# Performance work log

Measured on AMD Instinct MI355X. Metric: run time of the kernel, lower is better.

## Reference

```python
import jax, jax.numpy as jnp
import numpy as np

H = 8
D_MODEL = 512
NEG = -1e9  # fp32 masking value from the torch source


def setup_inputs() -> dict:
    key = jax.random.key(0)
    ks = jax.random.split(key, 13)
    B, T, C, D = 2, 512, 8, D_MODEL
    s = 1.0 / np.sqrt(D)
    inp = {
        "query": jax.random.normal(ks[0], (B, T, C, D), jnp.float32),
        "key": jax.random.normal(ks[1], (B, T, C, D), jnp.float32),
        "value": jax.random.normal(ks[2], (B, T, C, D), jnp.float32),
        "mask": jax.random.randint(ks[3], (B, T, T, 1), 0, 2, jnp.int32),
        # four Linear(d_model, d_model) layers, stored as (in, out)
        "Wq": jax.random.normal(ks[4], (D, D), jnp.float32) * s,
        "bq": jax.random.normal(ks[5], (D,), jnp.float32) * s,
        "Wk": jax.random.normal(ks[6], (D, D), jnp.float32) * s,
        "bk": jax.random.normal(ks[7], (D,), jnp.float32) * s,
        "Wv": jax.random.normal(ks[8], (D, D), jnp.float32) * s,
        "bv": jax.random.normal(ks[9], (D,), jnp.float32) * s,
        "Wo": jax.random.normal(ks[10], (D, D), jnp.float32) * s,
        "bo": jax.random.normal(ks[11], (D,), jnp.float32) * s,
    }
    return inp


def _mha(query, key, value, mask, Wq, bq, Wk, bk, Wv, bv, Wo, bo):
    B, T, C, D = query.shape
    h, dk = H, D // H

    def proj(x, W, b):
        y = (x @ W + b).reshape(B, T, C, h, dk)
        return jnp.transpose(y, (0, 3, 2, 1, 4))  # [B,h,C,T,dk] (torch transpose(1,3))

    q = proj(query, Wq, bq)
    k = proj(key, Wk, bk)
    v = proj(value, Wv, bv)

    scores = jnp.einsum("bhctd,bhcsd->bhcts", q, k) / np.sqrt(dk)  # [B,h,C,T,T]
    # The torch view/transpose/view dance is just a permutation putting C last;
    # it is equivalent to masking scores[b,h,c,t,s] where mask[b,t,s,0]==0
    # (mask broadcast over heads h and channels c).
    m = mask[:, :, :, 0]  # [B,T,Tk]
    scores = jnp.where(m[:, None, None, :, :] == 0, NEG, scores)
    p_attn = jax.nn.softmax(scores, axis=-1)
    # dropout omitted (inference/deterministic reference)
    x = jnp.einsum("bhcts,bhcsd->bhctd", p_attn, v)  # [B,h,C,T,dk]
    x = jnp.transpose(x, (0, 3, 2, 1, 4)).reshape(B, T, C, D)
    return x @ Wo + bo


def reference(query, key, value, mask, Wq, bq, Wk, bk, Wv, bv, Wo, bo):
    return _mha(query, key, value, mask, Wq, bq, Wk, bk, Wv, bv, Wo, bo)
```

## Files before the change

### kernel.cpp

```cpp
#include <hip/hip_runtime.h>
#include <hip/hip_bf16.h>

typedef __bf16 bf16;
typedef __bf16 bf16x8 __attribute__((ext_vector_type(8)));
typedef float floatx4 __attribute__((ext_vector_type(4)));


#define AS1 __attribute__((address_space(1)))
#define AS3 __attribute__((address_space(3)))

__device__ __forceinline__ void gload_lds16(const bf16* g, bf16* l) {
    __builtin_amdgcn_global_load_lds((const AS1 unsigned int*)g,
                                     (AS3 unsigned int*)l, 16, 0, 0);
}

union Pack8 { bf16 h[8]; uint4 u; };

__global__ __launch_bounds__(256) void wtr_kernel(
    const float* __restrict__ Wq, const float* __restrict__ Wk,
    const float* __restrict__ Wv, const float* __restrict__ Wo,
    bf16* __restrict__ WT)
{
    __shared__ float Ts[64][65];
    const int tid = threadIdx.x;
    const int k0 = blockIdx.x * 64;
    const int n0 = blockIdx.y * 64;
    const int z  = blockIdx.z;
    const float* W = (z == 0) ? Wq : (z == 1) ? Wk : (z == 2) ? Wv : Wo;
    bf16* O = WT + (size_t)z * 512 * 512;
    #pragma unroll
    for (int i = 0; i < 16; i++) {
        const int r = i * 4 + (tid >> 6), c = tid & 63;
        Ts[r][c] = W[(size_t)(k0 + r) * 512 + n0 + c];
    }
    __syncthreads();
    #pragma unroll
    for (int i = 0; i < 16; i++) {
        const int a = i * 4 + (tid >> 6), c = tid & 63;
        O[(size_t)(n0 + a) * 512 + k0 + c] = (bf16)Ts[c][a];
    }
}

__global__ __launch_bounds__(256) void gemm_qkv(
    const float* __restrict__ Aq, const float* __restrict__ Ak,
    const float* __restrict__ Av, const bf16* __restrict__ WT,
    const float* __restrict__ Bq, const float* __restrict__ Bk,
    const float* __restrict__ Bv,
    bf16* __restrict__ Oq, bf16* __restrict__ Ok, bf16* __restrict__ Ov)
{
    __shared__ bf16 Asm[128 * 32];
    __shared__ bf16 Bsm[128 * 32];
    __shared__ bf16 Tsm[128][136];
    const int z = blockIdx.z;
    const float* A    = (z == 0) ? Aq : (z == 1) ? Ak : Av;
    const float* bias = (z == 0) ? Bq : (z == 1) ? Bk : Bv;
    bf16* out         = (z == 0) ? Oq : (z == 1) ? Ok : Ov;
    const bf16* BT = WT + (size_t)z * 262144;
    const float scale = (z == 0) ? 0.125f : 1.0f;

    const int tid  = threadIdx.x;
    const int lane = tid & 63;
    const int wave = tid >> 6;
    const int quad = lane >> 4;
    const int l16  = lane & 15;
    const int mblk = blockIdx.x * 128;
    const int nblk = blockIdx.y * 128;

    const int srow = wave * 16 + (lane >> 2);
    const int scol = (lane & 3) * 8;
    const float* Ag0 = A + (size_t)(mblk + srow) * 512 + scol;
    const float* Ag1 = Ag0 + (size_t)64 * 512;
    const bf16* Bg0 = BT + (size_t)(nblk + srow) * 512 + scol;
    const bf16* Bg1 = Bg0 + (size_t)64 * 512;
    bf16* Alp0 = Asm + srow * 32 + scol;
    bf16* Alp1 = Alp0 + 64 * 32;
    bf16* Bl0 = Bsm + wave * 16 * 32;
    bf16* Bl1 = Bsm + (64 + wave * 16) * 32;

    const int wr = (wave >> 1) * 64;
    const int wc = (wave & 1) * 64;

    floatx4 acc[4][4] = {};
    for (int k0 = 0; k0 < 512; k0 += 32) {
        gload_lds16(Bg0 + k0, Bl0);
        gload_lds16(Bg1 + k0, Bl1);
        float4 x0 = *(const float4*)(Ag0 + k0);
        float4 x1 = *(const float4*)(Ag0 + k0 + 4);
        float4 y0 = *(const float4*)(Ag1 + k0);
        float4 y1 = *(const float4*)(Ag1 + k0 + 4);
        Pack8 pa, pb;
        pa.h[0] = (bf16)x0.x; pa.h[1] = (bf16)x0.y;
        pa.h[2] = (bf16)x0.z; pa.h[3] = (bf16)x0.w;
        pa.h[4] = (bf16)x1.x; pa.h[5] = (bf16)x1.y;
        pa.h[6] = (bf16)x1.z; pa.h[7] = (bf16)x1.w;
        pb.h[0] = (bf16)y0.x; pb.h[1] = (bf16)y0.y;
        pb.h[2] = (bf16)y0.z; pb.h[3] = (bf16)y0.w;
        pb.h[4] = (bf16)y1.x; pb.h[5] = (bf16)y1.y;
        pb.h[6] = (bf16)y1.z; pb.h[7] = (bf16)y1.w;
        *(uint4*)Alp0 = pa.u;
        *(uint4*)Alp1 = pb.u;
        __syncthreads();
        bf16x8 a[4], b[4];
        #pragma unroll
        for (int mt = 0; mt < 4; mt++)
            a[mt] = *(const bf16x8*)(Asm + (wr + mt * 16 + l16) * 32 + quad * 8);
        #pragma unroll
        for (int nt = 0; nt < 4; nt++)
            b[nt] = *(const bf16x8*)(Bsm + (wc + nt * 16 + l16) * 32 + quad * 8);
        #pragma unroll
        for (int mt = 0; mt < 4; mt++)
            #pragma unroll
            for (int nt = 0; nt < 4; nt++)
                acc[mt][nt] = __builtin_amdgcn_mfma_f32_16x16x32_bf16(
                    a[mt], b[nt], acc[mt][nt], 0, 0, 0);
        __syncthreads();
    }

    if (z != 2) {
        #pragma unroll
        for (int mt = 0; mt < 4; mt++) {
            #pragma unroll
            for (int nt = 0; nt < 4; nt++) {
                const int colg = nblk + wc + nt * 16 + l16;
                const float bb = bias[colg];
                #pragma unroll
                for (int r = 0; r < 4; r++) {
                    const int rowg = mblk + wr + mt * 16 + quad * 4 + r;
                    const float v = (acc[mt][nt][r] + bb) * scale;
                    const int b_ = rowg >> 12;
                    const int t_ = (rowg >> 3) & 511;
                    const int c  = rowg & 7;
                    const int h  = colg >> 6;
                    const int d  = colg & 63;
                    const int hd = b_ * 64 + h * 8 + c;
                    out[((size_t)hd * 512 + t_) * 64 + d] = (bf16)v;
                }
            }
        }
    } else {
        #pragma unroll
        for (int mt = 0; mt < 4; mt++) {
            #pragma unroll
            for (int nt = 0; nt < 4; nt++) {
                const int cl = wc + nt * 16 + l16;
                const float bb = bias[nblk + cl];
                #pragma unroll
                for (int r = 0; r < 4; r++)
                    Tsm[wr + mt * 16 + quad * 4 + r][cl] =
                        (bf16)(acc[mt][nt][r] + bb);
            }
        }
        __syncthreads();
        const int b_ = mblk >> 12;
        const int t0 = (mblk >> 3) & 511;
        #pragma unroll
        for (int ch = tid; ch < 1024; ch += 256) {
            const int col = ch >> 3, c = ch & 7;
            const int h = (nblk + col) >> 6, d = (nblk + col) & 63;
            const int hd = b_ * 64 + h * 8 + c;
            Pack8 lo, hi;
            #pragma unroll
            for (int j = 0; j < 8; j++) lo.h[j] = Tsm[j * 8 + c][col];
            #pragma unroll
            for (int j = 0; j < 8; j++) hi.h[j] = Tsm[(j + 8) * 8 + c][col];
            bf16* dst = out + ((size_t)hd * 64 + d) * 512 + t0;
            *(uint4*)dst = lo.u;
            *(uint4*)(dst + 8) = hi.u;
        }
    }
}

__global__ __launch_bounds__(256) void gemm_o(
    const bf16* __restrict__ A, const bf16* __restrict__ BT,
    const float* __restrict__ bias, float* __restrict__ out)
{
    __shared__ bf16 Asm[128 * 32];
    __shared__ bf16 Bsm[128 * 32];
    const int tid  = threadIdx.x;
    const int lane = tid & 63;
    const int wave = tid >> 6;
    const int quad = lane >> 4;
    const int l16  = lane & 15;
    const int mblk = blockIdx.x * 128;
    const int nblk = blockIdx.y * 128;

    const int srow = wave * 16 + (lane >> 2);
    const int scol = (lane & 3) * 8;
    const bf16* Ag0 = A + (size_t)(mblk + srow) * 512 + scol;
    const bf16* Ag1 = Ag0 + (size_t)64 * 512;
    const bf16* Bg0 = BT + (size_t)(nblk + srow) * 512 + scol;
    const bf16* Bg1 = Bg0 + (size_t)64 * 512;
    bf16* Al0 = Asm + wave * 16 * 32;
    bf16* Al1 = Asm + (64 + wave * 16) * 32;
    bf16* Bl0 = Bsm + wave * 16 * 32;
    bf16* Bl1 = Bsm + (64 + wave * 16) * 32;

    const int wr = (wave >> 1) * 64;
    const int wc = (wave & 1) * 64;

    floatx4 acc[4][4] = {};
    for (int k0 = 0; k0 < 512; k0 += 32) {
        gload_lds16(Ag0 + k0, Al0);
        gload_lds16(Ag1 + k0, Al1);
        gload_lds16(Bg0 + k0, Bl0);
        gload_lds16(Bg1 + k0, Bl1);
        __syncthreads();
        bf16x8 a[4], b[4];
        #pragma unroll
        for (int mt = 0; mt < 4; mt++)
            a[mt] = *(const bf16x8*)(Asm + (wr + mt * 16 + l16) * 32 + quad * 8);
        #pragma unroll
        for (int nt = 0; nt < 4; nt++)
            b[nt] = *(const bf16x8*)(Bsm + (wc + nt * 16 + l16) * 32 + quad * 8);
        #pragma unroll
        for (int mt = 0; mt < 4; mt++)
            #pragma unroll
            for (int nt = 0; nt < 4; nt++)
                acc[mt][nt] = __builtin_amdgcn_mfma_f32_16x16x32_bf16(
                    a[mt], b[nt], acc[mt][nt], 0, 0, 0);
        __syncthreads();
    }

    #pragma unroll
    for (int mt = 0; mt < 4; mt++) {
        #pragma unroll
        for (int nt = 0; nt < 4; nt++) {
            const int colg = nblk + wc + nt * 16 + l16;
            const float bb = bias[colg];
            #pragma unroll
            for (int r = 0; r < 4; r++) {
                const int rowg = mblk + wr + mt * 16 + quad * 4 + r;
                out[(size_t)rowg * 512 + colg] = acc[mt][nt][r] + bb;
            }
        }
    }
}

#define PST 520

__global__ __launch_bounds__(256, 2) void attn_kernel(
    const bf16* __restrict__ Qws, const bf16* __restrict__ Kws,
    const bf16* __restrict__ Vtws, const int* __restrict__ mask,
    bf16* __restrict__ Xws)
{
    __shared__ bf16 Psm[64][PST];
    __shared__ float redM[4][64];
    __shared__ float redS[4][64];
    const int tid  = threadIdx.x;
    const int wave = tid >> 6;
    const int lane = tid & 63;
    const int quad = lane >> 4;
    const int l16  = lane & 15;
    const int s_ = blockIdx.x;
    const int o_ = ((s_ & 7) << 7) | (s_ >> 3);
    const int hd = o_ >> 3;
    const int qt = o_ & 7;
    const int q0 = qt * 64;
    const int b = hd >> 6;
    const int h = (hd >> 3) & 7;
    const int c = hd & 7;

    const bf16* Qh = Qws + (size_t)hd * 512 * 64;
    const bf16* Kh = Kws + (size_t)hd * 512 * 64;
    const int* mp = mask + ((size_t)b * 512 + q0) * 512;

    bf16x8 aq[4][2];
    #pragma unroll
    for (int s = 0; s < 4; s++) {
        aq[s][0] = *(const bf16x8*)(Qh + (size_t)(q0 + s * 16 + l16) * 64 + quad * 8);
        aq[s][1] = *(const bf16x8*)(Qh + (size_t)(q0 + s * 16 + l16) * 64 + 32 + quad * 8);
    }

    floatx4 sv[4][8];
    #pragma unroll
    for (int s = 0; s < 4; s++)
        #pragma unroll
        for (int nt = 0; nt < 8; nt++)
            sv[s][nt] = (floatx4){0.f, 0.f, 0.f, 0.f};

    #pragma unroll
    for (int nt = 0; nt < 8; nt++) {
        const int s0 = wave * 128 + nt * 16;
        bf16x8 bk0 = *(const bf16x8*)(Kh + (size_t)(s0 + l16) * 64 + quad * 8);
        bf16x8 bk1 = *(const bf16x8*)(Kh + (size_t)(s0 + l16) * 64 + 32 + quad * 8);
        #pragma unroll
        for (int s = 0; s < 4; s++) {
            sv[s][nt] = __builtin_amdgcn_mfma_f32_16x16x32_bf16(
                aq[s][0], bk0, sv[s][nt], 0, 0, 0);
            sv[s][nt] = __builtin_amdgcn_mfma_f32_16x16x32_bf16(
                aq[s][1], bk1, sv[s][nt], 0, 0, 0);
        }
    }

    float mx[4][4];
    #pragma unroll
    for (int s = 0; s < 4; s++)
        #pragma unroll
        for (int r = 0; r < 4; r++)
            mx[s][r] = -3.0e38f;
    #pragma unroll
    for (int s = 0; s < 4; s++)
        #pragma unroll
        for (int nt = 0; nt < 8; nt++)
            #pragma unroll
            for (int r = 0; r < 4; r++) {
                const int mv = mp[(size_t)(s * 16 + quad * 4 + r) * 512 +
                                  wave * 128 + nt * 16 + l16];
                const float v = sv[s][nt][r] + ((mv == 0) ? -1.0e9f : 0.0f);
                sv[s][nt][r] = v;
                mx[s][r] = fmaxf(mx[s][r], v);
            }
    #pragma unroll
    for (int off = 1; off < 16; off <<= 1)
        #pragma unroll
        for (int s = 0; s < 4; s++)
            #pragma unroll
            for (int r = 0; r < 4; r++)
                mx[s][r] = fmaxf(mx[s][r], __shfl_xor(mx[s][r], off, 64));
    if (l16 == 0)
        #pragma unroll
        for (int s = 0; s < 4; s++)
            #pragma unroll
            for (int r = 0; r < 4; r++)
                redM[wave][s * 16 + quad * 4 + r] = mx[s][r];
    __syncthreads();

    float mf[4][4], sum[4][4];
    #pragma unroll
    for (int s = 0; s < 4; s++)
        #pragma unroll
        for (int r = 0; r < 4; r++) {
            const int qr = s * 16 + quad * 4 + r;
            mf[s][r] = fmaxf(fmaxf(redM[0][qr], redM[1][qr]),
                             fmaxf(redM[2][qr], redM[3][qr]));
            sum[s][r] = 0.f;
        }
    #pragma unroll
    for (int s = 0; s < 4; s++)
        #pragma unroll
        for (int nt = 0; nt < 8; nt++)
            #pragma unroll
            for (int r = 0; r < 4; r++) {
                const float e = __expf(sv[s][nt][r] - mf[s][r]);
                sv[s][nt][r] = e;
                sum[s][r] += e;
            }
    #pragma unroll
    for (int off = 1; off < 16; off <<= 1)
        #pragma unroll
        for (int s = 0; s < 4; s++)
            #pragma unroll
            for (int r = 0; r < 4; r++)
                sum[s][r] += __shfl_xor(sum[s][r], off, 64);
    if (l16 == 0)
        #pragma unroll
        for (int s = 0; s < 4; s++)
            #pragma unroll
            for (int r = 0; r < 4; r++)
                redS[wave][s * 16 + quad * 4 + r] = sum[s][r];
    __syncthreads();

    #pragma unroll
    for (int s = 0; s < 4; s++)
        #pragma unroll
        for (int r = 0; r < 4; r++) {
            const int qr = s * 16 + quad * 4 + r;
            const float inv = 1.f / (redS[0][qr] + redS[1][qr] +
                                     redS[2][qr] + redS[3][qr]);
            #pragma unroll
            for (int nt = 0; nt < 8; nt++)
                Psm[qr][wave * 128 + nt * 16 + l16] =
                    (bf16)(sv[s][nt][r] * inv);
        }
    __syncthreads();

    const bf16* Vh = Vtws + (size_t)hd * 64 * 512;
    const int d0 = wave * 16;
    floatx4 o[4] = {};
    #pragma unroll
    for (int ks = 0; ks < 16; ks++) {
        bf16x8 bv = *(const bf16x8*)(Vh + (size_t)(d0 + l16) * 512 + ks * 32 + quad * 8);
        #pragma unroll
        for (int rt = 0; rt < 4; rt++) {
            bf16x8 ap = *(const bf16x8*)(&Psm[rt * 16 + l16][ks * 32 + quad * 8]);
            o[rt] = __builtin_amdgcn_mfma_f32_16x16x32_bf16(ap, bv, o[rt], 0, 0, 0);
        }
    }
    #pragma unroll
    for (int rt = 0; rt < 4; rt++)
        #pragma unroll
        for (int r = 0; r < 4; r++) {
            const int q = q0 + rt * 16 + quad * 4 + r;
            const size_t row = ((size_t)b * 512 + q) * 8 + c;
            Xws[row * 512 + h * 64 + d0 + l16] = (bf16)o[rt][r];
        }
}

extern "C" void kernel_launch(void* const* d_in, const int* in_sizes, int n_in,
                              void* d_out, int out_size, void* d_ws, size_t ws_size,
                              hipStream_t stream)
{
    const float* qin  = (const float*)d_in[0];
    const float* kin  = (const float*)d_in[1];
    const float* vin  = (const float*)d_in[2];
    const int*   mask = (const int*)d_in[3];
    const float* Bq = (const float*)d_in[5];
    const float* Bk = (const float*)d_in[7];
    const float* Bv = (const float*)d_in[9];
    const float* Bo = (const float*)d_in[11];
    float* out = (float*)d_out;

    const size_t R = (size_t)8192 * 512;
    bf16* r0 = (bf16*)d_ws;
    bf16* r1 = r0 + R;
    bf16* r2 = r1 + R;
    bf16* r3 = r2 + R;
    bf16* WT = r3 + R;

    wtr_kernel<<<dim3(8, 8, 4), dim3(256), 0, stream>>>(
        (const float*)d_in[4], (const float*)d_in[6],
        (const float*)d_in[8], (const float*)d_in[10], WT);
    gemm_qkv<<<dim3(64, 4, 3), dim3(256), 0, stream>>>(
        qin, kin, vin, WT, Bq, Bk, Bv, r0, r1, r2);
    attn_kernel<<<dim3(1024), dim3(256), 0, stream>>>(
        r0, r1, r2, mask, r3);
    gemm_o<<<dim3(64, 4), dim3(256), 0, stream>>>(
        r3, WT + (size_t)3 * 262144, Bo, out);
}
```

Before: 204.3 us.

## Use 512-thread GEMM blocks and transpose score MFMA for vectorized mask loads

The QKV and output projection GEMMs now launch 512 threads (8 waves) per 128x128 tile, with each wave owning a 32x64 sub-tile and issuing one global load per operand per k-step. This halves per-thread accumulator registers and raises wave-level parallelism. In the attention kernel the score MFMA operands are swapped so each lane holds four consecutive key columns of one query row. That allows int4 mask loads, cheaper two-step shuffle reductions for max and sum, and 8-byte packed stores of probabilities to LDS. The cost is more threads contending for the same barriers in the GEMMs.

```diff
diff --git a/kernel.cpp b/kernel.cpp
--- a/kernel.cpp
+++ b/kernel.cpp
@@ -15,6 +15,7 @@
 }
 
 union Pack8 { bf16 h[8]; uint4 u; };
+union Pack4 { bf16 h[4]; unsigned long long u; };
 
 __global__ __launch_bounds__(256) void wtr_kernel(
     const float* __restrict__ Wq, const float* __restrict__ Wk,
@@ -41,7 +42,7 @@
     }
 }
 
-__global__ __launch_bounds__(256) void gemm_qkv(
+__global__ __launch_bounds__(512, 4) void gemm_qkv(
     const float* __restrict__ Aq, const float* __restrict__ Ak,
     const float* __restrict__ Av, const bf16* __restrict__ WT,
     const float* __restrict__ Bq, const float* __restrict__ Bk,
@@ -68,47 +69,35 @@
 
     const int srow = wave * 16 + (lane >> 2);
     const int scol = (lane & 3) * 8;
-    const float* Ag0 = A + (size_t)(mblk + srow) * 512 + scol;
-    const float* Ag1 = Ag0 + (size_t)64 * 512;
-    const bf16* Bg0 = BT + (size_t)(nblk + srow) * 512 + scol;
-    const bf16* Bg1 = Bg0 + (size_t)64 * 512;
-    bf16* Alp0 = Asm + srow * 32 + scol;
-    bf16* Alp1 = Alp0 + 64 * 32;
-    bf16* Bl0 = Bsm + wave * 16 * 32;
-    bf16* Bl1 = Bsm + (64 + wave * 16) * 32;
-
-    const int wr = (wave >> 1) * 64;
+    const float* Ag = A + (size_t)(mblk + srow) * 512 + scol;
+    const bf16* Bg  = BT + (size_t)(nblk + srow) * 512 + scol;
+    bf16* Alp = Asm + srow * 32 + scol;
+    bf16* Bl  = Bsm + wave * 16 * 32;
+
+    const int wr = (wave >> 1) * 32;
     const int wc = (wave & 1) * 64;
 
-    floatx4 acc[4][4] = {};
+    floatx4 acc[2][4] = {};
     for (int k0 = 0; k0 < 512; k0 += 32) {
-        gload_lds16(Bg0 + k0, Bl0);
-        gload_lds16(Bg1 + k0, Bl1);
-        float4 x0 = *(const float4*)(Ag0 + k0);
-        float4 x1 = *(const float4*)(Ag0 + k0 + 4);
-        float4 y0 = *(const float4*)(Ag1 + k0);
-        float4 y1 = *(const float4*)(Ag1 + k0 + 4);
-        Pack8 pa, pb;
+        gload_lds16(Bg + k0, Bl);
+        float4 x0 = *(const float4*)(Ag + k0);
+        float4 x1 = *(const float4*)(Ag + k0 + 4);
+        Pack8 pa;
         pa.h[0] = (bf16)x0.x; pa.h[1] = (bf16)x0.y;
         pa.h[2] = (bf16)x0.z; pa.h[3] = (bf16)x0.w;
         pa.h[4] = (bf16)x1.x; pa.h[5] = (bf16)x1.y;
         pa.h[6] = (bf16)x1.z; pa.h[7] = (bf16)x1.w;
-        pb.h[0] = (bf16)y0.x; pb.h[1] = (bf16)y0.y;
-        pb.h[2] = (bf16)y0.z; pb.h[3] = (bf16)y0.w;
-        pb.h[4] = (bf16)y1.x; pb.h[5] = (bf16)y1.y;
-        pb.h[6] = (bf16)y1.z; pb.h[7] = (bf16)y1.w;
-        *(uint4*)Alp0 = pa.u;
-        *(uint4*)Alp1 = pb.u;
+        *(uint4*)Alp = pa.u;
         __syncthreads();
-        bf16x8 a[4], b[4];
-        #pragma unroll
-        for (int mt = 0; mt < 4; mt++)
+        bf16x8 a[2], b[4];
+        #pragma unroll
+        for (int mt = 0; mt < 2; mt++)
             a[mt] = *(const bf16x8*)(Asm + (wr + mt * 16 + l16) * 32 + quad * 8);
         #pragma unroll
         for (int nt = 0; nt < 4; nt++)
             b[nt] = *(const bf16x8*)(Bsm + (wc + nt * 16 + l16) * 32 + quad * 8);
         #pragma unroll
-        for (int mt = 0; mt < 4; mt++)
+        for (int mt = 0; mt < 2; mt++)
             #pragma unroll
             for (int nt = 0; nt < 4; nt++)
                 acc[mt][nt] = __builtin_amdgcn_mfma_f32_16x16x32_bf16(
@@ -118,7 +107,7 @@
 
     if (z != 2) {
         #pragma unroll
-        for (int mt = 0; mt < 4; mt++) {
+        for (int mt = 0; mt < 2; mt++) {
             #pragma unroll
             for (int nt = 0; nt < 4; nt++) {
                 const int colg = nblk + wc + nt * 16 + l16;
@@ -139,7 +128,7 @@
         }
     } else {
         #pragma unroll
-        for (int mt = 0; mt < 4; mt++) {
+        for (int mt = 0; mt < 2; mt++) {
             #pragma unroll
             for (int nt = 0; nt < 4; nt++) {
                 const int cl = wc + nt * 16 + l16;
@@ -154,7 +143,7 @@
         const int b_ = mblk >> 12;
         const int t0 = (mblk >> 3) & 511;
         #pragma unroll
-        for (int ch = tid; ch < 1024; ch += 256) {
+        for (int ch = tid; ch < 1024; ch += 512) {
             const int col = ch >> 3, c = ch & 7;
             const int h = (nblk + col) >> 6, d = (nblk + col) & 63;
             const int hd = b_ * 64 + h * 8 + c;
@@ -170,7 +159,7 @@
     }
 }
 
-__global__ __launch_bounds__(256) void gemm_o(
+__global__ __launch_bounds__(512, 4) void gemm_o(
     const bf16* __restrict__ A, const bf16* __restrict__ BT,
     const float* __restrict__ bias, float* __restrict__ out)
 {
@@ -186,34 +175,28 @@
 
     const int srow = wave * 16 + (lane >> 2);
     const int scol = (lane & 3) * 8;
-    const bf16* Ag0 = A + (size_t)(mblk + srow) * 512 + scol;
-    const bf16* Ag1 = Ag0 + (size_t)64 * 512;
-    const bf16* Bg0 = BT + (size_t)(nblk + srow) * 512 + scol;
-    const bf16* Bg1 = Bg0 + (size_t)64 * 512;
-    bf16* Al0 = Asm + wave * 16 * 32;
-    bf16* Al1 = Asm + (64 + wave * 16) * 32;
-    bf16* Bl0 = Bsm + wave * 16 * 32;
-    bf16* Bl1 = Bsm + (64 + wave * 16) * 32;
-
-    const int wr = (wave >> 1) * 64;
+    const bf16* Ag = A + (size_t)(mblk + srow) * 512 + scol;
+    const bf16* Bg = BT + (size_t)(nblk + srow) * 512 + scol;
+    bf16* Al = Asm + wave * 16 * 32;
+    bf16* Bl = Bsm + wave * 16 * 32;
+
+    const int wr = (wave >> 1) * 32;
     const int wc = (wave & 1) * 64;
 
-    floatx4 acc[4][4] = {};
+    floatx4 acc[2][4] = {};
     for (int k0 = 0; k0 < 512; k0 += 32) {
-        gload_lds16(Ag0 + k0, Al0);
-        gload_lds16(Ag1 + k0, Al1);
-        gload_lds16(Bg0 + k0, Bl0);
-        gload_lds16(Bg1 + k0, Bl1);
+        gload_lds16(Ag + k0, Al);
+        gload_lds16(Bg + k0, Bl);
         __syncthreads();
-        bf16x8 a[4], b[4];
-        #pragma unroll
-        for (int mt = 0; mt < 4; mt++)
+        bf16x8 a[2], b[4];
+        #pragma unroll
+        for (int mt = 0; mt < 2; mt++)
             a[mt] = *(const bf16x8*)(Asm + (wr + mt * 16 + l16) * 32 + quad * 8);
         #pragma unroll
         for (int nt = 0; nt < 4; nt++)
             b[nt] = *(const bf16x8*)(Bsm + (wc + nt * 16 + l16) * 32 + quad * 8);
         #pragma unroll
-        for (int mt = 0; mt < 4; mt++)
+        for (int mt = 0; mt < 2; mt++)
             #pragma unroll
             for (int nt = 0; nt < 4; nt++)
                 acc[mt][nt] = __builtin_amdgcn_mfma_f32_16x16x32_bf16(
@@ -222,7 +205,7 @@
     }
 
     #pragma unroll
-    for (int mt = 0; mt < 4; mt++) {
+    for (int mt = 0; mt < 2; mt++) {
         #pragma unroll
         for (int nt = 0; nt < 4; nt++) {
             const int colg = nblk + wc + nt * 16 + l16;
@@ -286,91 +269,80 @@
         #pragma unroll
         for (int s = 0; s < 4; s++) {
             sv[s][nt] = __builtin_amdgcn_mfma_f32_16x16x32_bf16(
-                aq[s][0], bk0, sv[s][nt], 0, 0, 0);
+                bk0, aq[s][0], sv[s][nt], 0, 0, 0);
             sv[s][nt] = __builtin_amdgcn_mfma_f32_16x16x32_bf16(
-                aq[s][1], bk1, sv[s][nt], 0, 0, 0);
-        }
-    }
-
-    float mx[4][4];
+                bk1, aq[s][1], sv[s][nt], 0, 0, 0);
+        }
+    }
+
+    float mx[4] = {-3.0e38f, -3.0e38f, -3.0e38f, -3.0e38f};
     #pragma unroll
     for (int s = 0; s < 4; s++)
         #pragma unroll
-        for (int r = 0; r < 4; r++)
-            mx[s][r] = -3.0e38f;
+        for (int nt = 0; nt < 8; nt++) {
+            const int4 mv = *(const int4*)(
+                mp + (size_t)(s * 16 + l16) * 512 + wave * 128 + nt * 16 + quad * 4);
+            float v0 = sv[s][nt][0] + ((mv.x == 0) ? -1.0e9f : 0.0f);
+            float v1 = sv[s][nt][1] + ((mv.y == 0) ? -1.0e9f : 0.0f);
+            float v2 = sv[s][nt][2] + ((mv.z == 0) ? -1.0e9f : 0.0f);
+            float v3 = sv[s][nt][3] + ((mv.w == 0) ? -1.0e9f : 0.0f);
+            sv[s][nt][0] = v0; sv[s][nt][1] = v1;
+            sv[s][nt][2] = v2; sv[s][nt][3] = v3;
+            mx[s] = fmaxf(mx[s], fmaxf(fmaxf(v0, v1), fmaxf(v2, v3)));
+        }
+    #pragma unroll
+    for (int s = 0; s < 4; s++) {
+        mx[s] = fmaxf(mx[s], __shfl_xor(mx[s], 16, 64));
+        mx[s] = fmaxf(mx[s], __shfl_xor(mx[s], 32, 64));
+    }
+    if (quad == 0)
+        #pragma unroll
+        for (int s = 0; s < 4; s++) redM[wave][s * 16 + l16] = mx[s];
+    __syncthreads();
+
+    float mf[4], sum[4] = {0.f, 0.f, 0.f, 0.f};
+    #pragma unroll
+    for (int s = 0; s < 4; s++) {
+        const int qr = s * 16 + l16;
+        mf[s] = fmaxf(fmaxf(redM[0][qr], redM[1][qr]),
+                      fmaxf(redM[2][qr], redM[3][qr]));
+    }
     #pragma unroll
     for (int s = 0; s < 4; s++)
         #pragma unroll
         for (int nt = 0; nt < 8; nt++)
             #pragma unroll
             for (int r = 0; r < 4; r++) {
-                const int mv = mp[(size_t)(s * 16 + quad * 4 + r) * 512 +
-                                  wave * 128 + nt * 16 + l16];
-                const float v = sv[s][nt][r] + ((mv == 0) ? -1.0e9f : 0.0f);
-                sv[s][nt][r] = v;
-                mx[s][r] = fmaxf(mx[s][r], v);
+                const float e = __expf(sv[s][nt][r] - mf[s]);
+                sv[s][nt][r] = e;
+                sum[s] += e;
             }
     #pragma unroll
-    for (int off = 1; off < 16; off <<= 1)
-        #pragma unroll
-        for (int s = 0; s < 4; s++)
+    for (int s = 0; s < 4; s++) {
+        sum[s] += __shfl_xor(sum[s], 16, 64);
+        sum[s] += __shfl_xor(sum[s], 32, 64);
+    }
+    if (quad == 0)
+        #pragma unroll
+        for (int s = 0; s < 4; s++) redS[wave][s * 16 + l16] = sum[s];
+    __syncthreads();
+
+    float inv[4];
+    #pragma unroll
+    for (int s = 0; s < 4; s++) {
+        const int qr = s * 16 + l16;
+        inv[s] = 1.f / (redS[0][qr] + redS[1][qr] + redS[2][qr] + redS[3][qr]);
+    }
+    #pragma unroll
+    for (int s = 0; s < 4; s++)
+        #pragma unroll
+        for (int nt = 0; nt < 8; nt++) {
+            Pack4 pk;
             #pragma unroll
             for (int r = 0; r < 4; r++)
-                mx[s][r] = fmaxf(mx[s][r], __shfl_xor(mx[s][r], off, 64));
-    if (l16 == 0)
-        #pragma unroll
-        for (int s = 0; s < 4; s++)
-            #pragma unroll
-            for (int r = 0; r < 4; r++)
-                redM[wave][s * 16 + quad * 4 + r] = mx[s][r];
-    __syncthreads();
-
-    float mf[4][4], sum[4][4];
-    #pragma unroll
-    for (int s = 0; s < 4; s++)
-        #pragma unroll
-        for (int r = 0; r < 4; r++) {
-            const int qr = s * 16 + quad * 4 + r;
-            mf[s][r] = fmaxf(fmaxf(redM[0][qr], redM[1][qr]),
-                             fmaxf(redM[2][qr], redM[3][qr]));
-            sum[s][r] = 0.f;
-        }
-    #pragma unroll
-    for (int s = 0; s < 4; s++)
-        #pragma unroll
-        for (int nt = 0; nt < 8; nt++)
-            #pragma unroll
-            for (int r = 0; r < 4; r++) {
-                const float e = __expf(sv[s][nt][r] - mf[s][r]);
-                sv[s][nt][r] = e;
-                sum[s][r] += e;
-            }
-    #pragma unroll
-    for (int off = 1; off < 16; off <<= 1)
-        #pragma unroll
-        for (int s = 0; s < 4; s++)
-            #pragma unroll
-            for (int r = 0; r < 4; r++)
-                sum[s][r] += __shfl_xor(sum[s][r], off, 64);
-    if (l16 == 0)
-        #pragma unroll
-        for (int s = 0; s < 4; s++)
-            #pragma unroll
-            for (int r = 0; r < 4; r++)
-                redS[wave][s * 16 + quad * 4 + r] = sum[s][r];
-    __syncthreads();
-
-    #pragma unroll
-    for (int s = 0; s < 4; s++)
-        #pragma unroll
-        for (int r = 0; r < 4; r++) {
-            const int qr = s * 16 + quad * 4 + r;
-            const float inv = 1.f / (redS[0][qr] + redS[1][qr] +
-                                     redS[2][qr] + redS[3][qr]);
-            #pragma unroll
-            for (int nt = 0; nt < 8; nt++)
-                Psm[qr][wave * 128 + nt * 16 + l16] =
-                    (bf16)(sv[s][nt][r] * inv);
+                pk.h[r] = (bf16)(sv[s][nt][r] * inv[s]);
+            *(unsigned long long*)&Psm[s * 16 + l16][wave * 128 + nt * 16 + quad * 4]
+                = pk.u;
         }
     __syncthreads();
 
@@ -420,10 +392,10 @@
     wtr_kernel<<<dim3(8, 8, 4), dim3(256), 0, stream>>>(
         (const float*)d_in[4], (const float*)d_in[6],
         (const float*)d_in[8], (const float*)d_in[10], WT);
-    gemm_qkv<<<dim3(64, 4, 3), dim3(256), 0, stream>>>(
+    gemm_qkv<<<dim3(64, 4, 3), dim3(512), 0, stream>>>(
         qin, kin, vin, WT, Bq, Bk, Bv, r0, r1, r2);
     attn_kernel<<<dim3(1024), dim3(256), 0, stream>>>(
         r0, r1, r2, mask, r3);
-    gemm_o<<<dim3(64, 4), dim3(256), 0, stream>>>(
+    gemm_o<<<dim3(64, 4), dim3(512), 0, stream>>>(
         r3, WT + (size_t)3 * 262144, Bo, out);
 }
```

Result: faster. 193.5 us (-5.3%).
